# Kernel optimization log

Measured on AMD Instinct MI355X. Metric: run time of the kernel, lower is better.

## Reference

```python
import jax, jax.numpy as jnp
import numpy as np

H = 20      # LSTM hidden size (hard-coded in module)
FF = 64     # linear1 out
B = 131072  # batch
T = 256     # input_length


def _init_lstm(key, in_dim, hid):
    k1, k2, k3, k4 = jax.random.split(key, 4)
    s = 1.0 / np.sqrt(hid)
    return (
        jax.random.uniform(k1, (4 * hid, in_dim), jnp.float32, -s, s),
        jax.random.uniform(k2, (4 * hid, hid), jnp.float32, -s, s),
        jax.random.uniform(k3, (4 * hid,), jnp.float32, -s, s),
        jax.random.uniform(k4, (4 * hid,), jnp.float32, -s, s),
    )


def setup_inputs() -> dict:
    key = jax.random.key(0)
    ks = jax.random.split(key, 7)
    diagnosis = jax.random.normal(ks[0], (B, T), jnp.float32)
    W_ih1, W_hh1, b_ih1, b_hh1 = _init_lstm(ks[1], 1, H)
    W_ih2, W_hh2, b_ih2, b_hh2 = _init_lstm(ks[2], H, H)
    s1 = 1.0 / np.sqrt(H)
    W1 = jax.random.uniform(ks[3], (FF, H), jnp.float32, -s1, s1)
    b1 = jax.random.uniform(ks[4], (FF,), jnp.float32, -s1, s1)
    s2 = 1.0 / np.sqrt(FF)
    W2 = jax.random.uniform(ks[5], (1, FF), jnp.float32, -s2, s2)
    b2 = jax.random.uniform(ks[6], (1,), jnp.float32, -s2, s2)
    return {"diagnosis": diagnosis,
            "W_ih1": W_ih1, "W_hh1": W_hh1, "b_ih1": b_ih1, "b_hh1": b_hh1,
            "W_ih2": W_ih2, "W_hh2": W_hh2, "b_ih2": b_ih2, "b_hh2": b_hh2,
            "W1": W1, "b1": b1, "W2": W2, "b2": b2}


def _lstm_cell(x, h, c, W_ih, W_hh, b_ih, b_hh):
    # PyTorch LSTMCell gate ordering: i, f, g, o
    z = x @ W_ih.T + h @ W_hh.T + b_ih + b_hh  # [B, 4H]
    i, f, g, o = jnp.split(z, 4, axis=-1)
    c_new = jax.nn.sigmoid(f) * c + jax.nn.sigmoid(i) * jnp.tanh(g)
    h_new = jax.nn.sigmoid(o) * jnp.tanh(c_new)
    return h_new, c_new


def reference(diagnosis, W_ih1, W_hh1, b_ih1, b_hh1,
              W_ih2, W_hh2, b_ih2, b_hh2, W1, b1, W2, b2):
    bsz = diagnosis.shape[0]
    xs = diagnosis.T[:, :, None]  # [T, B, 1]
    zeros = jnp.zeros((bsz, H), diagnosis.dtype)

    def step(carry, x_t):
        h1, c1, h2, c2 = carry
        h1, c1 = _lstm_cell(x_t, h1, c1, W_ih1, W_hh1, b_ih1, b_hh1)
        h2, c2 = _lstm_cell(h1, h2, c2, W_ih2, W_hh2, b_ih2, b_hh2)
        return (h1, c1, h2, c2), None

    (h1, c1, h2, c2), _ = jax.lax.scan(step, (zeros, zeros, zeros, zeros), xs)
    y1 = jax.nn.relu(h2 @ W1.T + b1)
    y2 = jax.nn.relu(y1 @ W2.T + b2)  # [B, 1]
    return y2
```

## Files before the change

### kernel.cpp

```cpp
#include <hip/hip_runtime.h>

#define HH 20
#define TSTEPS 256
#define FF 64
#define EPW 64
#define ROWLEN 72
#define LOG2E 1.44269504088896f

typedef __attribute__((ext_vector_type(8))) _Float16 f16x8;
typedef __attribute__((ext_vector_type(2))) _Float16 f16x2;
typedef __attribute__((ext_vector_type(4))) float    f32x4;
typedef __attribute__((ext_vector_type(2))) float    f32x2;

__device__ __forceinline__ f32x4 mfma16(f16x8 a, f16x8 b, f32x4 c) {
    return __builtin_amdgcn_mfma_f32_16x16x32_f16(a, b, c, 0, 0, 0);
}
__device__ __forceinline__ float rcpf(float x) { return __builtin_amdgcn_rcpf(x); }
__device__ __forceinline__ float exp2fast(float x) {
#if __has_builtin(__builtin_amdgcn_exp2f)
    return __builtin_amdgcn_exp2f(x);
#else
    return __expf(x * 0.6931471805599453f);
#endif
}

__device__ __forceinline__ f32x2 act_pair(f32x4 za, f32x4 zb, f32x2& c) {
    f32x2 ei; ei.x = exp2fast(za.x); ei.y = exp2fast(zb.x);
    f32x2 ef; ef.x = exp2fast(za.y); ef.y = exp2fast(zb.y);
    f32x2 eg; eg.x = exp2fast(za.z); eg.y = exp2fast(zb.z);
    f32x2 eo; eo.x = exp2fast(za.w); eo.y = exp2fast(zb.w);
    const f32x2 one = {1.0f, 1.0f};
    f32x2 rf; rf.x = rcpf(1.0f + ef.x); rf.y = rcpf(1.0f + ef.y);
    f32x2 den1 = (one + ei) * (one + eg);
    f32x2 r1; r1.x = rcpf(den1.x); r1.y = rcpf(den1.y);
    c = c * rf + (eg - one) * r1;
    f32x2 sc = c * (2.0f * LOG2E);
    sc.x = fminf(sc.x, 100.0f); sc.y = fminf(sc.y, 100.0f);
    f32x2 ec; ec.x = exp2fast(sc.x); ec.y = exp2fast(sc.y);
    f32x2 den2 = (one + eo) * (one + ec);
    f32x2 r2; r2.x = rcpf(den2.x); r2.y = rcpf(den2.y);
    return (ec - one) * r2;
}
__device__ __forceinline__ float act_one(f32x4 za, float& c) {
    float ei = exp2fast(za.x), ef = exp2fast(za.y);
    float eg = exp2fast(za.z), eo = exp2fast(za.w);
    float rf = rcpf(1.0f + ef);
    float r1 = rcpf((1.0f + ei) * (1.0f + eg));
    c = c * rf + (eg - 1.0f) * r1;
    float sc = fminf(c * (2.0f * LOG2E), 100.0f);
    float ec = exp2fast(sc);
    float r2 = rcpf((1.0f + eo) * (1.0f + ec));
    return (ec - 1.0f) * r2;
}

__global__ void prep_weights(
    const float* __restrict__ Wih1, const float* __restrict__ Whh1,
    const float* __restrict__ bih1, const float* __restrict__ bhh1,
    const float* __restrict__ Wih2, const float* __restrict__ Whh2,
    const float* __restrict__ bih2, const float* __restrict__ bhh2,
    _Float16* __restrict__ ws)
{
    const int t0 = blockIdx.x * blockDim.x + threadIdx.x;
    const int stride = blockDim.x * gridDim.x;
    for (int idx = t0; idx < 80 * 32; idx += stride) {
        int r = idx >> 5, k = idx & 31;
        int m = r >> 4, q = (r >> 2) & 3, g = r & 3;
        int u = 5 * q + m, ro = g * HH + u;
        float s = (g == 2) ? 2.0f * LOG2E : -LOG2E;
        float v = 0.0f;
        if (k < 24)       { int qc = k / 6, wc = k % 6; if (wc < 5) v = Whh1[ro * HH + 5 * qc + wc]; }
        else if (k == 24)   v = Wih1[ro];
        else if (k == 25)   v = bih1[ro] + bhh1[ro];
        ws[idx] = (_Float16)(s * v);
    }
    for (int idx = t0; idx < 80 * 64; idx += stride) {
        int r = idx >> 6, k = idx & 63;
        int m = r >> 4, q = (r >> 2) & 3, g = r & 3;
        int u = 5 * q + m, ro = g * HH + u;
        float s = (g == 2) ? 2.0f * LOG2E : -LOG2E;
        float v = 0.0f;
        if (k < 24)       { int qc = k / 6, wc = k % 6; if (wc < 5) v = Wih2[ro * HH + 5 * qc + wc]; }
        else if (k == 25)   v = bih2[ro] + bhh2[ro];
        else if (k >= 26 && k < 50) {
            int cH = k - 26, qc = cH / 6, wc = cH % 6;
            if (wc < 5) v = Whh2[ro * HH + 5 * qc + wc];
        }
        ws[2560 + idx] = (_Float16)(s * v);
    }
}

__global__ __launch_bounds__(64, 2) void lstm_mfma(
    const float* __restrict__ diag,
    const _Float16* __restrict__ wpk,
    const float* __restrict__ W1, const float* __restrict__ b1,
    const float* __restrict__ W2, const float* __restrict__ b2,
    float* __restrict__ out, int Btot)
{
    __shared__ _Float16 s_B[EPW * ROWLEN];

    const int lane = threadIdx.x;
    const int q  = lane >> 4;
    const int cc = lane & 15;
    const int e  = blockIdx.x * EPW + lane;
    const int esafe = (e < Btot) ? e : (Btot - 1);

    {
        uint4 zz = {0u, 0u, 0u, 0u};
        #pragma unroll
        for (int j = 0; j < 9; ++j)
            *(uint4*)((char*)s_B + lane * 144 + j * 16) = zz;
    }

    f16x8 A1[5], A2a[5], A2b[5];
    {
        const _Float16* W2c = wpk + 2560;
        const int kb = q * 8;
        #pragma unroll
        for (int m = 0; m < 5; ++m) {
            const int r = 16 * m + cc;
            A1[m]  = *(const f16x8*)(wpk + r * 32 + kb);
            A2a[m] = *(const f16x8*)(W2c + r * 64 + kb);
            A2b[m] = *(const f16x8*)(W2c + r * 64 + 32 + kb);
        }
    }

    f32x2 c1p[4][2], c2p[4][2];
    float c1s[4], c2s[4];
    #pragma unroll
    for (int n = 0; n < 4; ++n) {
        c1p[n][0] = (f32x2){0.0f, 0.0f}; c1p[n][1] = (f32x2){0.0f, 0.0f};
        c2p[n][0] = (f32x2){0.0f, 0.0f}; c2p[n][1] = (f32x2){0.0f, 0.0f};
        c1s[n] = 0.0f; c2s[n] = 0.0f;
    }

    const float* __restrict__ xr = diag + (long long)esafe * TSTEPS;
    float x = xr[0];
    const f32x4 zz4 = {0.0f, 0.0f, 0.0f, 0.0f};

    #pragma unroll 1
    for (int t = 0; t < TSTEPS; ++t) {
        float xn = xr[(t + 1) & (TSTEPS - 1)];

        {
            f16x2 pk; pk.x = (_Float16)x; pk.y = (_Float16)1.0f;
            *(f16x2*)(s_B + lane * ROWLEN + 24) = pk;
        }

        #pragma unroll
        for (int n = 0; n < 4; ++n) {
            const _Float16* rowp = s_B + (n * 16 + cc) * ROWLEN;
            f16x8 bf = *(const f16x8*)(rowp + 8 * q);
            f32x4 z0 = mfma16(A1[0], bf, zz4);
            f32x4 z1 = mfma16(A1[1], bf, zz4);
            f32x4 z2 = mfma16(A1[2], bf, zz4);
            f32x4 z3 = mfma16(A1[3], bf, zz4);
            f32x4 z4 = mfma16(A1[4], bf, zz4);
            _Float16* wp = s_B + (n * 16 + cc) * ROWLEN + 6 * q;
            f32x2 h01 = act_pair(z0, z1, c1p[n][0]);
            { f16x2 o; o.x = (_Float16)h01.x; o.y = (_Float16)h01.y; *(f16x2*)(wp) = o; }
            f32x2 h23 = act_pair(z2, z3, c1p[n][1]);
            { f16x2 o; o.x = (_Float16)h23.x; o.y = (_Float16)h23.y; *(f16x2*)(wp + 2) = o; }
            float h4 = act_one(z4, c1s[n]);
            wp[4] = (_Float16)h4;
        }

        #pragma unroll
        for (int n = 0; n < 4; ++n) {
            const _Float16* rowp = s_B + (n * 16 + cc) * ROWLEN;
            f16x8 b0  = *(const f16x8*)(rowp + 8 * q);
            f16x8 b1f = *(const f16x8*)(rowp + 32 + 8 * q);
            f32x4 z0 = mfma16(A2b[0], b1f, mfma16(A2a[0], b0, zz4));
            f32x4 z1 = mfma16(A2b[1], b1f, mfma16(A2a[1], b0, zz4));
            f32x4 z2 = mfma16(A2b[2], b1f, mfma16(A2a[2], b0, zz4));
            f32x4 z3 = mfma16(A2b[3], b1f, mfma16(A2a[3], b0, zz4));
            f32x4 z4 = mfma16(A2b[4], b1f, mfma16(A2a[4], b0, zz4));
            _Float16* wp = s_B + (n * 16 + cc) * ROWLEN + 26 + 6 * q;
            f32x2 h01 = act_pair(z0, z1, c2p[n][0]);
            { f16x2 o; o.x = (_Float16)h01.x; o.y = (_Float16)h01.y; *(f16x2*)(wp) = o; }
            f32x2 h23 = act_pair(z2, z3, c2p[n][1]);
            { f16x2 o; o.x = (_Float16)h23.x; o.y = (_Float16)h23.y; *(f16x2*)(wp + 2) = o; }
            float h4 = act_one(z4, c2s[n]);
            wp[4] = (_Float16)h4;
        }

        x = xn;
    }

    if (e < Btot) {
        const _Float16* rowp = s_B + lane * ROWLEN + 26;
        float hv[HH];
        #pragma unroll
        for (int qq = 0; qq < 4; ++qq)
            #pragma unroll
            for (int ww = 0; ww < 5; ++ww)
                hv[5 * qq + ww] = (float)rowp[6 * qq + ww];

        float y2 = b2[0];
        #pragma unroll 1
        for (int jj = 0; jj < FF; ++jj) {
            float a = b1[jj];
            const float* __restrict__ wj = W1 + jj * HH;
            #pragma unroll
            for (int k = 0; k < HH; ++k)
                a = fmaf(hv[k], wj[k], a);
            a = fmaxf(a, 0.0f);
            y2 = fmaf(a, W2[jj], y2);
        }
        out[e] = fmaxf(y2, 0.0f);
    }
}

extern "C" void kernel_launch(void* const* d_in, const int* in_sizes, int n_in,
                              void* d_out, int out_size, void* d_ws, size_t ws_size,
                              hipStream_t stream)
{
    (void)n_in; (void)ws_size; (void)out_size;
    const float* diag = (const float*)d_in[0];
    const float* Wih1 = (const float*)d_in[1];
    const float* Whh1 = (const float*)d_in[2];
    const float* bih1 = (const float*)d_in[3];
    const float* bhh1 = (const float*)d_in[4];
    const float* Wih2 = (const float*)d_in[5];
    const float* Whh2 = (const float*)d_in[6];
    const float* bih2 = (const float*)d_in[7];
    const float* bhh2 = (const float*)d_in[8];
    const float* W1   = (const float*)d_in[9];
    const float* b1   = (const float*)d_in[10];
    const float* W2   = (const float*)d_in[11];
    const float* b2   = (const float*)d_in[12];

    const int Btot = in_sizes[0] / TSTEPS;
    _Float16* wpk = (_Float16*)d_ws;

    prep_weights<<<8, 256, 0, stream>>>(Wih1, Whh1, bih1, bhh1,
                                        Wih2, Whh2, bih2, bhh2, wpk);

    lstm_mfma<<<(Btot + EPW - 1) / EPW, 64, 0, stream>>>(
        diag, wpk, W1, b1, W2, b2, (float*)d_out, Btot);
}
```

Measured before the change: 1.317 ms.

## Halve elements per wave and merge LSTM cell-state reciprocals

Each 64-thread block now handles 32 batch elements (two 16-column MFMA tiles) instead of 64, doubling the grid and raising the launch-bounds occupancy hint from 2 to 4 waves. The aim is more concurrent waves to hide the serial latency of the MFMA and activation chain in each timestep, at the cost of half the lanes doing idle loads and the extra per-element work in the final MLP. Separately, the cell-state update combines the two reciprocals into one by putting both terms over a common denominator. That saves a transcendental per gate pair but adds a few multiplies and carries a slight overflow risk in the product denominator.

```diff
diff --git a/kernel.cpp b/kernel.cpp
--- a/kernel.cpp
+++ b/kernel.cpp
@@ -3,7 +3,8 @@
 #define HH 20
 #define TSTEPS 256
 #define FF 64
-#define EPW 64
+#define EPW 32
+#define NB 2
 #define ROWLEN 72
 #define LOG2E 1.44269504088896f
 
@@ -30,10 +31,12 @@
     f32x2 eg; eg.x = exp2fast(za.z); eg.y = exp2fast(zb.z);
     f32x2 eo; eo.x = exp2fast(za.w); eo.y = exp2fast(zb.w);
     const f32x2 one = {1.0f, 1.0f};
-    f32x2 rf; rf.x = rcpf(1.0f + ef.x); rf.y = rcpf(1.0f + ef.y);
-    f32x2 den1 = (one + ei) * (one + eg);
-    f32x2 r1; r1.x = rcpf(den1.x); r1.y = rcpf(den1.y);
-    c = c * rf + (eg - one) * r1;
+    f32x2 P = (one + ei) * (one + eg);
+    f32x2 Q = one + ef;
+    f32x2 num = c * P + (eg - one) * Q;
+    f32x2 den = P * Q;
+    f32x2 r; r.x = rcpf(den.x); r.y = rcpf(den.y);
+    c = num * r;
     f32x2 sc = c * (2.0f * LOG2E);
     sc.x = fminf(sc.x, 100.0f); sc.y = fminf(sc.y, 100.0f);
     f32x2 ec; ec.x = exp2fast(sc.x); ec.y = exp2fast(sc.y);
@@ -44,9 +47,10 @@
 __device__ __forceinline__ float act_one(f32x4 za, float& c) {
     float ei = exp2fast(za.x), ef = exp2fast(za.y);
     float eg = exp2fast(za.z), eo = exp2fast(za.w);
-    float rf = rcpf(1.0f + ef);
-    float r1 = rcpf((1.0f + ei) * (1.0f + eg));
-    c = c * rf + (eg - 1.0f) * r1;
+    float P = (1.0f + ei) * (1.0f + eg);
+    float Q = 1.0f + ef;
+    float num = fmaf(c, P, (eg - 1.0f) * Q);
+    c = num * rcpf(P * Q);
     float sc = fminf(c * (2.0f * LOG2E), 100.0f);
     float ec = exp2fast(sc);
     float r2 = rcpf((1.0f + eo) * (1.0f + ec));
@@ -89,7 +93,7 @@
     }
 }
 
-__global__ __launch_bounds__(64, 2) void lstm_mfma(
+__global__ __launch_bounds__(64, 4) void lstm_mfma(
     const float* __restrict__ diag,
     const _Float16* __restrict__ wpk,
     const float* __restrict__ W1, const float* __restrict__ b1,
@@ -101,10 +105,10 @@
     const int lane = threadIdx.x;
     const int q  = lane >> 4;
     const int cc = lane & 15;
-    const int e  = blockIdx.x * EPW + lane;
+    const int e  = blockIdx.x * EPW + (lane & (EPW - 1));
     const int esafe = (e < Btot) ? e : (Btot - 1);
 
-    {
+    if (lane < EPW) {
         uint4 zz = {0u, 0u, 0u, 0u};
         #pragma unroll
         for (int j = 0; j < 9; ++j)
@@ -124,10 +128,10 @@
         }
     }
 
-    f32x2 c1p[4][2], c2p[4][2];
-    float c1s[4], c2s[4];
+    f32x2 c1p[NB][2], c2p[NB][2];
+    float c1s[NB], c2s[NB];
     #pragma unroll
-    for (int n = 0; n < 4; ++n) {
+    for (int n = 0; n < NB; ++n) {
         c1p[n][0] = (f32x2){0.0f, 0.0f}; c1p[n][1] = (f32x2){0.0f, 0.0f};
         c2p[n][0] = (f32x2){0.0f, 0.0f}; c2p[n][1] = (f32x2){0.0f, 0.0f};
         c1s[n] = 0.0f; c2s[n] = 0.0f;
@@ -141,13 +145,13 @@
     for (int t = 0; t < TSTEPS; ++t) {
         float xn = xr[(t + 1) & (TSTEPS - 1)];
 
-        {
+        if (lane < EPW) {
             f16x2 pk; pk.x = (_Float16)x; pk.y = (_Float16)1.0f;
             *(f16x2*)(s_B + lane * ROWLEN + 24) = pk;
         }
 
         #pragma unroll
-        for (int n = 0; n < 4; ++n) {
+        for (int n = 0; n < NB; ++n) {
             const _Float16* rowp = s_B + (n * 16 + cc) * ROWLEN;
             f16x8 bf = *(const f16x8*)(rowp + 8 * q);
             f32x4 z0 = mfma16(A1[0], bf, zz4);
@@ -165,7 +169,7 @@
         }
 
         #pragma unroll
-        for (int n = 0; n < 4; ++n) {
+        for (int n = 0; n < NB; ++n) {
             const _Float16* rowp = s_B + (n * 16 + cc) * ROWLEN;
             f16x8 b0  = *(const f16x8*)(rowp + 8 * q);
             f16x8 b1f = *(const f16x8*)(rowp + 32 + 8 * q);
@@ -186,7 +190,7 @@
         x = xn;
     }
 
-    if (e < Btot) {
+    if (lane < EPW && e < Btot) {
         const _Float16* rowp = s_B + lane * ROWLEN + 26;
         float hv[HH];
         #pragma unroll
```

After: 1.277 ms. 3.1% less time.
